# Optimization experiments

Hardware: AMD Instinct MI355X
Metric: run time of the kernel (lower is better)

The kernel has to match this reference:

```python
import jax, jax.numpy as jnp
import numpy as np

SIGMA_MIN, SIGMA_MAX = 0.03, 0.35
LAMBDA_GEO = 8.0
COMPAT_SCALE = 0.1
INVALID_W = 0.05
NH, HD = 8, 64
LN_EPS = 1e-5

def _ln(x, g, b):
    m = x.mean(-1, keepdims=True)
    v = ((x - m) ** 2).mean(-1, keepdims=True)
    return (x - m) * jax.lax.rsqrt(v + LN_EPS) * g + b

def setup_inputs() -> dict:
    key = jax.random.key(0)
    ks = jax.random.split(key, 32)
    B, C, H, W = 8, 512, 32, 32
    T, S, D, SIN = 1024, 1024, 512, 512
    s = 0.02
    inp = {
        'front_feat': jax.random.normal(ks[0], (B, C, H, W), jnp.float32),
        'sat_tokens': jax.random.normal(ks[1], (B, S, SIN), jnp.float32),
        'sat_xy': jax.random.uniform(ks[2], (B, S, 2), jnp.float32),
        'front_bev_xy': jax.random.uniform(ks[3], (B, T, 2), jnp.float32),
        'front_bev_valid_mask': jax.random.bernoulli(ks[4], 0.9, (B, T)),
        'front_plucker': jax.random.normal(ks[5], (B, T, 6), jnp.float32),
        'fa_w': jax.random.normal(ks[6], (C, D), jnp.float32) * s,
        'fa_b': jnp.zeros((D,), jnp.float32),
        'fa_g': jnp.ones((D,), jnp.float32),
        'fa_lb': jnp.zeros((D,), jnp.float32),
        'sa_w': jax.random.normal(ks[7], (SIN, D), jnp.float32) * s,
        'sa_b': jnp.zeros((D,), jnp.float32),
        'sa_g': jnp.ones((D,), jnp.float32),
        'sa_lb': jnp.zeros((D,), jnp.float32),
        'q_w': jax.random.normal(ks[8], (D, D), jnp.float32) * s,
        'q_b': jnp.zeros((D,), jnp.float32),
        'k_w': jax.random.normal(ks[9], (D, D), jnp.float32) * s,
        'k_b': jnp.zeros((D,), jnp.float32),
        'v_w': jax.random.normal(ks[10], (D, D), jnp.float32) * s,
        'v_b': jnp.zeros((D,), jnp.float32),
        'pl_w1': jax.random.normal(ks[11], (6, D), jnp.float32) * s,
        'pl_b1': jnp.zeros((D,), jnp.float32),
        'pl_w2': jax.random.normal(ks[12], (D, D), jnp.float32) * s,
        'pl_b2': jnp.zeros((D,), jnp.float32),
        'sig_w': jax.random.normal(ks[13], (D, 1), jnp.float32) * s,
        'sig_b': jnp.zeros((1,), jnp.float32),
        'db_w': jax.random.normal(ks[14], (D, NH), jnp.float32) * s,
        'db_b': jnp.zeros((NH,), jnp.float32),
        'out_w': jax.random.normal(ks[15], (D, C), jnp.float32) * s,
        'out_b': jnp.zeros((C,), jnp.float32),
    }
    return inp

def _forward(front_feat, sat_tokens, sat_xy, front_bev_xy, front_plucker,
             fa_w, fa_b, fa_g, fa_lb, sa_w, sa_b, sa_g, sa_lb,
             q_w, q_b, k_w, k_b, v_w, v_b, pl_w1, pl_b1, pl_w2, pl_b2,
             sig_w, sig_b, db_w, db_b, out_w, out_b, valid_mask):
    B, C, H, W = front_feat.shape
    T = H * W
    D = NH * HD
    front_flat = front_feat.reshape(B, C, T).transpose(0, 2, 1)  # [B,T,C]
    front_embed = _ln(front_flat @ fa_w + fa_b, fa_g, fa_lb)
    pl = jax.nn.silu(front_plucker @ pl_w1 + pl_b1) @ pl_w2 + pl_b2
    context = front_embed + pl
    sat_embed = _ln(sat_tokens @ sa_w + sa_b, sa_g, sa_lb)
    def heads(x):
        return x.reshape(B, -1, NH, HD).transpose(0, 2, 1, 3)  # [B,H,N,d]
    q = heads(front_embed @ q_w + q_b)
    k = heads(sat_embed @ k_w + k_b)
    v = heads(sat_embed @ v_w + v_b)
    compat = jnp.einsum('bhtd,bhsd->bhts', q, k) / jnp.sqrt(jnp.float32(HD))
    compat = COMPAT_SCALE * compat
    sigma = SIGMA_MIN + (SIGMA_MAX - SIGMA_MIN) * jax.nn.sigmoid((context @ sig_w + sig_b)[..., 0])  # [B,T]
    dist2 = ((front_bev_xy[:, :, None, :] - sat_xy[:, None, :, :]) ** 2).sum(-1)  # [B,T,S]
    geo = -LAMBDA_GEO * dist2 / jnp.maximum(sigma[..., None] ** 2, 1e-6)
    sat_logits = compat + geo[:, None]  # [B,H,T,S]
    sat_logits = jnp.where(valid_mask[:, None, :, None], sat_logits, jnp.float32(-10000.0))
    dustbin = (context @ db_w + db_b).transpose(0, 2, 1)[..., None]  # [B,H,T,1]
    logits = jnp.concatenate([sat_logits, dustbin], axis=-1)
    probs = jax.nn.softmax(logits, axis=-1)
    sat_probs, dustbin_prob = probs[..., :-1], probs[..., -1]
    read = jnp.einsum('bhts,bhsd->bhtd', sat_probs, v)
    read = read.transpose(0, 2, 1, 3).reshape(B, T, D)
    read_feat = (read @ out_w + out_b).transpose(0, 2, 1).reshape(B, C, H, W)
    confidence = (1.0 - dustbin_prob).mean(axis=1)  # [B,T]
    conf_feat = confidence.reshape(B, 1, H, W)
    front_feat_out = front_feat + conf_feat * read_feat
    vf = valid_mask.astype(confidence.dtype)
    inv = 1.0 - vf
    invalid_conf = (confidence * inv).sum() / jnp.maximum(inv.sum(), 1.0)
    invalid_conf_loss = invalid_conf * INVALID_W
    return front_feat_out, read_feat, confidence, invalid_conf_loss

def reference(front_feat, sat_tokens, sat_xy, front_bev_xy, front_bev_valid_mask, front_plucker,
              fa_w, fa_b, fa_g, fa_lb, sa_w, sa_b, sa_g, sa_lb,
              q_w, q_b, k_w, k_b, v_w, v_b, pl_w1, pl_b1, pl_w2, pl_b2,
              sig_w, sig_b, db_w, db_b, out_w, out_b):
    return _forward(front_feat, sat_tokens, sat_xy, front_bev_xy, front_plucker,
                    fa_w, fa_b, fa_g, fa_lb, sa_w, sa_b, sa_g, sa_lb,
                    q_w, q_b, k_w, k_b, v_w, v_b, pl_w1, pl_b1, pl_w2, pl_b2,
                    sig_w, sig_b, db_w, db_b, out_w, out_b, front_bev_valid_mask)
```

## Files before the change

kernel.cpp:

```cpp
#include <hip/hip_runtime.h>

typedef unsigned short u16;
typedef __attribute__((ext_vector_type(8))) short short8;
typedef __attribute__((ext_vector_type(4))) float f32x4;

constexpr int B_  = 8;
constexpr int C_  = 512;
constexpr int T_  = 1024;
constexpr int S_  = 1024;
constexpr int D_  = 512;
constexpr int NH_ = 8;
constexpr int BT_ = B_ * T_;
constexpr float INVLN2 = 1.44269504088896340736f;
constexpr float QSCALE2 = 0.0125f * INVLN2;

__device__ __forceinline__ unsigned pack2(float lo, float hi) {
    unsigned r;
    asm("v_cvt_pk_bf16_f32 %0, %1, %2" : "=v"(r) : "v"(lo), "v"(hi));
    return r;
}
__device__ __forceinline__ u16 f2bf(float x) {
    return (u16)pack2(x, x);
}
__device__ __forceinline__ float bf2f(u16 h) {
    union { unsigned u; float f; } v; v.u = ((unsigned)h) << 16;
    return v.f;
}
__device__ __forceinline__ float fexp2(float x) {
    float r;
    asm("v_exp_f32 %0, %1" : "=v"(r) : "v"(x));
    return r;
}
__device__ __forceinline__ float max3f(float a, float b, float c) {
    float r;
    asm("v_max3_f32 %0, %1, %2, %3" : "=v"(r) : "v"(a), "v"(b), "v"(c));
    return r;
}

#define GWAITBAR(N) do { \
    asm volatile("s_waitcnt vmcnt(" #N ") lgkmcnt(0)" ::: "memory"); \
    __builtin_amdgcn_sched_barrier(0); \
    __builtin_amdgcn_s_barrier(); \
    __builtin_amdgcn_sched_barrier(0); } while (0)

typedef __attribute__((address_space(3))) unsigned int lds_u32;
typedef const __attribute__((address_space(1))) unsigned int glob_u32;
__device__ __forceinline__ void g2l16(void* l, const void* g) {
    __builtin_amdgcn_global_load_lds((glob_u32*)g, (lds_u32*)l, 16, 0, 0);
}

__device__ __forceinline__ int is_valid(const void* mask, int mode, int idx) {
    if (mode == 0) return ((const int*)mask)[idx] != 0;
    if (mode == 1) return ((const float*)mask)[idx] != 0.0f;
    return ((const unsigned char*)mask)[idx] != 0;
}

__global__ __launch_bounds__(256) void prep_k(
    const float* __restrict__ ff, const float* __restrict__ sat,
    const float* __restrict__ pl,
    const float* a0, const float* a1, const float* a2, const float* a3,
    const float* a4, const float* a5, const float* a6, u16* __restrict__ WT,
    u16* __restrict__ ffb, u16* __restrict__ satb,
    const float* __restrict__ plw1, const float* __restrict__ plb1,
    u16* __restrict__ plh,
    const unsigned* __restrict__ maskw, int* __restrict__ mode,
    float* __restrict__ scal) {
    __shared__ float tile[32][33];
    int blk = blockIdx.x, tid = threadIdx.x;
    if (blk < 4096) {
        int t0 = (blk & 31) * 32, c0 = ((blk >> 5) & 15) * 32, b = blk >> 9;
        int tx = tid & 31, ty = tid >> 5;
        const float* ip = ff + (size_t)b * C_ * T_;
        for (int i = ty; i < 32; i += 8)
            tile[i][tx] = ip[(size_t)(c0 + i) * T_ + t0 + tx];
        __syncthreads();
        u16* op = ffb + (size_t)b * T_ * C_;
        for (int i = ty; i < 32; i += 8)
            op[(size_t)(t0 + i) * C_ + c0 + tx] = f2bf(tile[tx][i]);
    } else if (blk < 5888) {
        int idx = blk - 4096;
        const float* srcs[7] = {a0, a1, a2, a3, a4, a5, a6};
        int z = idx >> 8;
        const float* src = srcs[z];
        u16* d = WT + (size_t)z * 512 * 512;
        int k0 = (idx & 15) * 32, n0 = ((idx >> 4) & 15) * 32;
        int tx = tid & 31, ty = tid >> 5;
        for (int i = ty; i < 32; i += 8)
            tile[i][tx] = src[(size_t)(k0 + i) * 512 + n0 + tx];
        __syncthreads();
        for (int i = ty; i < 32; i += 8)
            d[(size_t)(n0 + i) * 512 + k0 + tx] = f2bf(tile[tx][i]);
    } else if (blk < 7936) {
        int i = (blk - 5888) * 256 + tid;
        const float4* p = (const float4*)(sat + (size_t)i * 8);
        float4 a = p[0], b = p[1];
        uint4 o;
        o.x = pack2(a.x, a.y); o.y = pack2(a.z, a.w);
        o.z = pack2(b.x, b.y); o.w = pack2(b.z, b.w);
        *(uint4*)(satb + (size_t)i * 8) = o;
    } else if (blk < 9984) {
        int m = (blk - 7936) * 4 + (tid >> 6);
        int lane = tid & 63;
        float p6[6];
#pragma unroll
        for (int j = 0; j < 6; ++j) p6[j] = pl[(size_t)m * 6 + j];
        int n0 = lane * 8;
        float acc[8];
#pragma unroll
        for (int e = 0; e < 8; ++e) acc[e] = plb1[n0 + e];
#pragma unroll
        for (int j = 0; j < 6; ++j) {
            float4 wv0 = *(const float4*)(plw1 + j * D_ + n0);
            float4 wv1 = *(const float4*)(plw1 + j * D_ + n0 + 4);
            acc[0] += p6[j] * wv0.x; acc[1] += p6[j] * wv0.y;
            acc[2] += p6[j] * wv0.z; acc[3] += p6[j] * wv0.w;
            acc[4] += p6[j] * wv1.x; acc[5] += p6[j] * wv1.y;
            acc[6] += p6[j] * wv1.z; acc[7] += p6[j] * wv1.w;
        }
        uint4 o;
        float s0 = acc[0] / (1.0f + __expf(-acc[0]));
        float s1 = acc[1] / (1.0f + __expf(-acc[1]));
        float s2 = acc[2] / (1.0f + __expf(-acc[2]));
        float s3 = acc[3] / (1.0f + __expf(-acc[3]));
        float s4 = acc[4] / (1.0f + __expf(-acc[4]));
        float s5 = acc[5] / (1.0f + __expf(-acc[5]));
        float s6 = acc[6] / (1.0f + __expf(-acc[6]));
        float s7 = acc[7] / (1.0f + __expf(-acc[7]));
        o.x = pack2(s0, s1); o.y = pack2(s2, s3);
        o.z = pack2(s4, s5); o.w = pack2(s6, s7);
        *(uint4*)(plh + (size_t)m * D_ + n0) = o;
    } else {
        __shared__ int bad_i, bad_f;
        if (tid == 0) { bad_i = 0; bad_f = 0; }
        __syncthreads();
        for (int i = tid; i < 2048; i += 256) {
            unsigned v = maskw[i];
            if (v > 1u) bad_i = 1;
            if (v != 0u && v != 0x3f800000u) bad_f = 1;
        }
        __syncthreads();
        if (tid == 0) {
            *mode = (!bad_i) ? 0 : ((!bad_f) ? 1 : 2);
            scal[0] = 0.0f; scal[1] = 0.0f;
        }
    }
}

__global__ __launch_bounds__(256) void gmm_k(
    const u16* __restrict__ A0, const u16* __restrict__ A1,
    const u16* __restrict__ A2, const u16* __restrict__ A3,
    const u16* __restrict__ Bt0, const u16* __restrict__ Bt1,
    const u16* __restrict__ Bt2, const u16* __restrict__ Bt3,
    const float* __restrict__ bb0, const float* __restrict__ bb1,
    const float* __restrict__ bb2, const float* __restrict__ bb3,
    void* __restrict__ C0v, void* __restrict__ C1v,
    void* __restrict__ C2v, void* __restrict__ C3v,
    int md0, int md1, int md2, int md3,
    const u16* __restrict__ addend,
    const float* __restrict__ ffp, float* __restrict__ out1p,
    const float* __restrict__ dbpp, const void* __restrict__ maskp,
    const int* __restrict__ modep, float* __restrict__ outcp,
    float* __restrict__ scalp) {
    __shared__ u16 As[3][4096];
    __shared__ u16 Bs[3][4096];
    __shared__ float confL[128];
    int jid = blockIdx.x >> 8;
    int L = blockIdx.x & 255;
    const u16* A    = (jid == 0) ? A0 : (jid == 1) ? A1 : (jid == 2) ? A2 : A3;
    const u16* Bt   = (jid == 0) ? Bt0 : (jid == 1) ? Bt1 : (jid == 2) ? Bt2 : Bt3;
    const float* bias = (jid == 0) ? bb0 : (jid == 1) ? bb1 : (jid == 2) ? bb2 : bb3;
    void* Cv        = (jid == 0) ? C0v : (jid == 1) ? C1v : (jid == 2) ? C2v : C3v;
    int mode        = (jid == 0) ? md0 : (jid == 1) ? md1 : (jid == 2) ? md2 : md3;

    int tid = threadIdx.x, w = tid >> 6, l = tid & 63;
    int lr = l & 15, g = l >> 4;
    int W = (L & 7) * 32 + (L >> 3);
    int m0 = (W >> 2) * 128, n0 = (W & 3) * 128;
    int wr = w >> 1, wc = w & 1;
    int prm = g ^ ((lr >> 1) & 3);

    f32x4 acc[4][4] = {};

    if (mode == 4 && tid < 128) {
        int row = m0 + tid;
        const float* dr = dbpp + (size_t)row * NH_;
        float s = 0;
#pragma unroll
        for (int h = 0; h < 8; ++h) s += dr[h];
        float cf = 1.0f - s * 0.125f;
        confL[tid] = cf;
        if ((W & 3) == 0) {
            outcp[row] = cf;
            int md = *modep;
            float invd = is_valid(maskp, md, row) ? 0.0f : 1.0f;
            float a = cf * invd, bsum = invd;
            for (int o = 32; o; o >>= 1) {
                a += __shfl_down(a, o);
                bsum += __shfl_down(bsum, o);
            }
            if ((tid & 63) == 0) {
                atomicAdd(&scalp[0], a);
                atomicAdd(&scalp[1], bsum);
            }
        }
    }

    auto stage = [&](int buf, int k0) {
#pragma unroll
        for (int j = 0; j < 2; ++j) {
            int i = tid + 256 * j;
            int row = i >> 2, gg = (i & 3) ^ ((i >> 3) & 3);
            g2l16((char*)As[buf] + (size_t)i * 16,
                  A + (size_t)(m0 + row) * 512 + k0 + gg * 8);
        }
#pragma unroll
        for (int j = 0; j < 2; ++j) {
            int i = tid + 256 * j;
            int col = i >> 2, gg = (i & 3) ^ ((i >> 3) & 3);
            g2l16((char*)Bs[buf] + (size_t)i * 16,
                  Bt + (size_t)(n0 + col) * 512 + k0 + gg * 8);
        }
    };

    auto compute = [&](int bi) {
        const char* Ab = (const char*)As[bi];
        const char* Bb = (const char*)Bs[bi];
        short8 af[4], bf[4];
#pragma unroll
        for (int m = 0; m < 4; ++m)
            af[m] = *(const short8*)(Ab + ((wr * 64 + m * 16 + lr) * 4 + prm) * 16);
#pragma unroll
        for (int n = 0; n < 4; ++n)
            bf[n] = *(const short8*)(Bb + ((wc * 64 + n * 16 + lr) * 4 + prm) * 16);
        __builtin_amdgcn_s_setprio(1);
#pragma unroll
        for (int m = 0; m < 4; ++m)
#pragma unroll
            for (int n = 0; n < 4; ++n)
                acc[m][n] = __builtin_amdgcn_mfma_f32_16x16x32_bf16(
                    af[m], bf[n], acc[m][n], 0, 0, 0);
        __builtin_amdgcn_s_setprio(0);
    };

    stage(0, 0);
    stage(1, 32);
    for (int t = 0; t < 14; ++t) {
        stage((t + 2) % 3, (t + 2) * 32);
        GWAITBAR(8);
        compute(t % 3);
        __builtin_amdgcn_s_barrier();
    }
    GWAITBAR(4);
    compute(2);
    GWAITBAR(0);
    compute(0);

    float bs[4];
#pragma unroll
    for (int n = 0; n < 4; ++n) bs[n] = bias[n0 + wc * 64 + n * 16 + lr];

#pragma unroll
    for (int m = 0; m < 4; ++m) {
#pragma unroll
        for (int n = 0; n < 4; ++n) {
            int R0  = m0 + wr * 64 + m * 16 + 4 * g;
            int col = n0 + wc * 64 + n * 16 + lr;
            if (mode == 3) {
                int bbx = R0 >> 10, ss = R0 & 1023, hh = col >> 6, dd = col & 63;
                uint2 pk;
                pk.x = pack2(acc[m][n][0] + bs[n], acc[m][n][1] + bs[n]);
                pk.y = pack2(acc[m][n][2] + bs[n], acc[m][n][3] + bs[n]);
                u16* dst = (u16*)Cv + ((size_t)(bbx * 8 + hh) * 64 + dd) * 1024 + ss;
                *(uint2*)dst = pk;
            } else if (mode == 4) {
                int bbx = R0 >> 10, t0p = R0 & 1023;
                size_t base = (size_t)bbx * C_ * T_ + (size_t)col * T_ + t0p;
                float4 rf;
                rf.x = acc[m][n][0] + bs[n]; rf.y = acc[m][n][1] + bs[n];
                rf.z = acc[m][n][2] + bs[n]; rf.w = acc[m][n][3] + bs[n];
                float4 ffv = *(const float4*)(ffp + base);
                float4 cfv = *(const float4*)&confL[R0 - m0];
                float4 o0v;
                o0v.x = ffv.x + cfv.x * rf.x; o0v.y = ffv.y + cfv.y * rf.y;
                o0v.z = ffv.z + cfv.z * rf.z; o0v.w = ffv.w + cfv.w * rf.w;
                *(float4*)(out1p + base) = rf;
                *(float4*)((float*)Cv + base) = o0v;
            } else {
#pragma unroll
                for (int j = 0; j < 4; ++j) {
                    int row = R0 + j;
                    float v = acc[m][n][j] + bs[n];
                    if (mode == 1) v *= QSCALE2;
                    if (mode == 2) v += bf2f(addend[(size_t)row * 512 + col]);
                    ((u16*)Cv)[(size_t)row * 512 + col] = f2bf(v);
                }
            }
        }
    }
}

__global__ __launch_bounds__(256) void ln2_k(
    const u16* __restrict__ X0, const float* __restrict__ g0,
    const float* __restrict__ b0, u16* __restrict__ O0,
    const u16* __restrict__ X1, const float* __restrict__ g1,
    const float* __restrict__ b1, u16* __restrict__ O1) {
    int sel = blockIdx.x >> 13;
    int row = blockIdx.x & 8191;
    const u16* X = sel ? X1 : X0;
    const float* gw = sel ? g1 : g0;
    const float* bw = sel ? b1 : b0;
    u16* out = sel ? O1 : O0;
    int tid = threadIdx.x;
    const unsigned* xr = (const unsigned*)(X + (size_t)row * D_);
    unsigned u = xr[tid];
    float x0 = bf2f((u16)(u & 0xffff)), x1 = bf2f((u16)(u >> 16));
    float s = x0 + x1, sq = x0 * x0 + x1 * x1;
    __shared__ float rs[4], rq[4];
    for (int o = 32; o; o >>= 1) { s += __shfl_down(s, o); sq += __shfl_down(sq, o); }
    int wid = tid >> 6, lane = tid & 63;
    if (lane == 0) { rs[wid] = s; rq[wid] = sq; }
    __syncthreads();
    if (tid == 0) {
        float ts = 0, tq = 0;
        for (int w = 0; w < 4; ++w) { ts += rs[w]; tq += rq[w]; }
        rs[0] = ts; rq[0] = tq;
    }
    __syncthreads();
    float mean = rs[0] * (1.0f / D_);
    float var  = rq[0] * (1.0f / D_) - mean * mean;
    float r = rsqrtf(var + 1e-5f);
    float2 g2 = *(const float2*)(gw + 2 * tid);
    float2 b2 = *(const float2*)(bw + 2 * tid);
    float y0 = (x0 - mean) * r * g2.x + b2.x;
    float y1 = (x1 - mean) * r * g2.y + b2.y;
    ((unsigned*)(out + (size_t)row * D_))[tid] = pack2(y0, y1);
}

__global__ __launch_bounds__(256) void head_k(const u16* __restrict__ ctx,
        const float* __restrict__ sw, const float* __restrict__ sbb,
        const float* __restrict__ dw, const float* __restrict__ dbb,
        float* __restrict__ sig, float* __restrict__ dbo) {
    int w = threadIdx.x >> 6, lane = threadIdx.x & 63;
    int row = blockIdx.x * 4 + w;
    const u16* xr = ctx + (size_t)row * D_;
    short8 xv = *(const short8*)(xr + lane * 8);
    float xs[8];
#pragma unroll
    for (int i = 0; i < 8; ++i) xs[i] = bf2f((u16)xv[i]);
    float4 wa = *(const float4*)(sw + lane * 8);
    float4 wb = *(const float4*)(sw + lane * 8 + 4);
    float sacc = xs[0] * wa.x + xs[1] * wa.y + xs[2] * wa.z + xs[3] * wa.w +
                 xs[4] * wb.x + xs[5] * wb.y + xs[6] * wb.z + xs[7] * wb.w;
    float d_[8] = {};
    const float* dr = dw + (size_t)lane * 8 * NH_;
#pragma unroll
    for (int i = 0; i < 8; ++i)
#pragma unroll
        for (int hh = 0; hh < 8; ++hh) d_[hh] += xs[i] * dr[i * NH_ + hh];
    for (int o = 32; o; o >>= 1) {
        sacc += __shfl_down(sacc, o);
#pragma unroll
        for (int hh = 0; hh < 8; ++hh) d_[hh] += __shfl_down(d_[hh], o);
    }
    if (lane == 0) {
        float z = sacc + sbb[0];
        sig[row] = 0.03f + 0.32f / (1.0f + __expf(-z));
        float* dd = dbo + (size_t)row * NH_;
#pragma unroll
        for (int hh = 0; hh < 8; ++hh) dd[hh] = d_[hh] + dbb[hh];
    }
}

__global__ __launch_bounds__(512) void attn_k(
    const u16* __restrict__ Q, const u16* __restrict__ K,
    const u16* __restrict__ Vt, const float* __restrict__ sig,
    const float* __restrict__ dbl, const float* __restrict__ bev,
    const float* __restrict__ sxy, const void* __restrict__ mask,
    const int* __restrict__ mode, u16* __restrict__ OUT,
    float* __restrict__ dbp) {
    int L = blockIdx.x;
    int W = (L & 7) * 64 + (L >> 3);
    int b = W >> 6, h = (W >> 3) & 7, tblk = W & 7;
    int tid = threadIdx.x, w = tid >> 6, l = tid & 63;
    int lr = l & 15, g = l >> 4;
    int p8 = lr & 7;

    __shared__ u16 Kbuf[2][4096];
    __shared__ u16 Vbuf[2][4096];
    __shared__ float2 SXY[1024];
    __shared__ float  SZ[1024];

    const float2* xp = (const float2*)(sxy + (size_t)b * S_ * 2);
#pragma unroll
    for (int j = 0; j < 2; ++j) {
        int idx = tid + 512 * j;
        float2 v = xp[idx];
        SXY[idx] = make_float2(-2.0f * v.x, -2.0f * v.y);
        SZ[idx] = v.x * v.x + v.y * v.y;
    }

    int trow = b * T_ + tblk * 128 + w * 16 + lr;
    float s_ = sig[trow];
    float bx = bev[(size_t)trow * 2], by = bev[(size_t)trow * 2 + 1];
    float dbv2 = dbl[(size_t)trow * NH_ + h] * INVLN2;
    int md = *mode;
    bool vld = is_valid(mask, md, trow) != 0;
    float grow  = vld ? (-11.5415603271117f / fmaxf(s_ * s_, 1e-6f)) : 0.0f;
    float Abase = vld ? grow * (bx * bx + by * by) : -10000.0f;
    float AbaseM = Abase - dbv2;
    float mshift = 0.0f;

    const u16* qp = Q + (size_t)trow * 512 + h * 64 + g * 8;
    short8 q0 = *(const short8*)qp;
    short8 q1 = *(const short8*)(qp + 32);
    if (!vld) { q0 = short8{}; q1 = short8{}; }

    short8 ones;
#pragma unroll
    for (int e = 0; e < 8; ++e) ones[e] = (short)0x3F80;

    const u16* Kp = K + (size_t)b * S_ * 512 + h * 64;
    const u16* Vp = Vt + (size_t)(b * 8 + h) * 64 * 1024;

    int srow = tid >> 3;
    int gprm = (tid & 7) ^ (srow & 7);
    int sK = ((srow >> 5) & 1) * 32 + ((srow >> 2) & 3) * 8 +
             ((srow >> 4) & 1) * 4 + (srow & 3);

    auto stageKV = [&](int buf, int s0) {
        g2l16((char*)Kbuf[buf] + (size_t)tid * 16,
              Kp + (size_t)(s0 + sK) * 512 + gprm * 8);
        g2l16((char*)Vbuf[buf] + (size_t)tid * 16,
              Vp + (size_t)srow * 1024 + s0 + gprm * 8);
    };

    f32x4 o0 = {}, o1 = {}, o2 = {}, o3 = {};
    f32x4 o4 = {1.0f, 1.0f, 1.0f, 1.0f};

    stageKV(0, 0);
    int cur = 0;
    for (int c = 0; c < 16; ++c) {
        int s0c = c * 64;
        if (c < 15) {
            stageKV(cur ^ 1, s0c + 64);
            GWAITBAR(2);
        } else {
            GWAITBAR(0);
        }

        const char* Kc = (const char*)Kbuf[cur];
        const char* Vc = (const char*)Vbuf[cur];

        f32x4 p[4];
        f32x4 z4 = {};
        __builtin_amdgcn_s_setprio(1);
#pragma unroll
        for (int sub = 0; sub < 4; ++sub) {
            int krow = sub * 16 + lr;
            short8 kf0 = *(const short8*)(Kc + (krow * 8 + (g ^ p8)) * 16);
            short8 kf1 = *(const short8*)(Kc + (krow * 8 + ((4 + g) ^ p8)) * 16);
            p[sub] = __builtin_amdgcn_mfma_f32_16x16x32_bf16(kf0, q0, z4, 0, 0, 0);
            p[sub] = __builtin_amdgcn_mfma_f32_16x16x32_bf16(kf1, q1, p[sub], 0, 0, 0);
        }
        __builtin_amdgcn_s_setprio(0);

        float lg[16];
#pragma unroll
        for (int sub = 0; sub < 4; ++sub) {
            int sl = s0c + ((sub & 2) << 4) + 8 * g + ((sub & 1) << 2);
            float4 xy01 = *(const float4*)&SXY[sl];
            float4 xy23 = *(const float4*)&SXY[sl + 2];
            float4 zz   = *(const float4*)&SZ[sl];
            float X[4] = {xy01.x, xy01.z, xy23.x, xy23.z};
            float Y[4] = {xy01.y, xy01.w, xy23.y, xy23.w};
            float Z[4] = {zz.x, zz.y, zz.z, zz.w};
#pragma unroll
            for (int i2 = 0; i2 < 4; ++i2) {
                float wg = fmaf(bx, X[i2], fmaf(by, Y[i2], Z[i2]));
                lg[sub * 4 + i2] = fmaf(grow, wg, p[sub][i2] + AbaseM);
            }
        }
        float c0 = max3f(lg[0], lg[1], lg[2]);
        float c1 = max3f(lg[3], lg[4], lg[5]);
        float c2 = max3f(lg[6], lg[7], lg[8]);
        float c3 = max3f(lg[9], lg[10], lg[11]);
        float c4 = max3f(lg[12], lg[13], lg[14]);
        float cl = fmaxf(max3f(c0, c1, c2), max3f(c3, c4, lg[15]));

        if (!__all(cl <= 11.5f)) {
            cl = fmaxf(cl, __shfl_xor(cl, 16));
            cl = fmaxf(cl, __shfl_xor(cl, 32));
            float dm = fmaxf(cl, 0.0f);
            float scl = fexp2(-dm);
            o0 *= scl; o1 *= scl; o2 *= scl; o3 *= scl; o4 *= scl;
            AbaseM -= dm;
            mshift -= dm;
#pragma unroll
            for (int r = 0; r < 16; ++r) lg[r] -= dm;
        }
        float pe[16];
#pragma unroll
        for (int r = 0; r < 16; ++r) pe[r] = fexp2(lg[r]);

        union { uint4 u; short8 s8; } pf0, pf1;
        pf0.u.x = pack2(pe[0], pe[1]);  pf0.u.y = pack2(pe[2], pe[3]);
        pf0.u.z = pack2(pe[4], pe[5]);  pf0.u.w = pack2(pe[6], pe[7]);
        pf1.u.x = pack2(pe[8], pe[9]);  pf1.u.y = pack2(pe[10], pe[11]);
        pf1.u.z = pack2(pe[12], pe[13]); pf1.u.w = pack2(pe[14], pe[15]);

        __builtin_amdgcn_s_setprio(1);
        short8 vf;
#pragma unroll
        for (int dt = 0; dt < 4; ++dt) {
            int vrow = dt * 16 + lr;
            f32x4* oo = (dt == 0) ? &o0 : (dt == 1) ? &o1 : (dt == 2) ? &o2 : &o3;
            vf = *(const short8*)(Vc + (vrow * 8 + (g ^ p8)) * 16);
            *oo = __builtin_amdgcn_mfma_f32_16x16x32_bf16(vf, pf0.s8, *oo, 0, 0, 0);
            vf = *(const short8*)(Vc + (vrow * 8 + ((4 + g) ^ p8)) * 16);
            *oo = __builtin_amdgcn_mfma_f32_16x16x32_bf16(vf, pf1.s8, *oo, 0, 0, 0);
        }
        o4 = __builtin_amdgcn_mfma_f32_16x16x32_bf16(ones, pf0.s8, o4, 0, 0, 0);
        o4 = __builtin_amdgcn_mfma_f32_16x16x32_bf16(ones, pf1.s8, o4, 0, 0, 0);
        __builtin_amdgcn_s_setprio(0);

        __builtin_amdgcn_s_barrier();
        cur ^= 1;
    }

    float inv = 1.0f / o4[0];
    u16* ob = OUT + (size_t)trow * 512 + h * 64;
    {
        uint2 pk;
        pk.x = pack2(o0[0] * inv, o0[1] * inv); pk.y = pack2(o0[2] * inv, o0[3] * inv);
        *(uint2*)(ob + 0 * 16 + 4 * g) = pk;
        pk.x = pack2(o1[0] * inv, o1[1] * inv); pk.y = pack2(o1[2] * inv, o1[3] * inv);
        *(uint2*)(ob + 1 * 16 + 4 * g) = pk;
        pk.x = pack2(o2[0] * inv, o2[1] * inv); pk.y = pack2(o2[2] * inv, o2[3] * inv);
        *(uint2*)(ob + 2 * 16 + 4 * g) = pk;
        pk.x = pack2(o3[0] * inv, o3[1] * inv); pk.y = pack2(o3[2] * inv, o3[3] * inv);
        *(uint2*)(ob + 3 * 16 + 4 * g) = pk;
    }
    if (g == 0) dbp[(size_t)trow * NH_ + h] = fexp2(mshift) * inv;
}

__global__ void loss_k(const float* __restrict__ scal, float* __restrict__ out) {
    out[0] = scal[0] / fmaxf(scal[1], 1.0f) * 0.05f;
}

extern "C" void kernel_launch(void* const* d_in, const int* in_sizes, int n_in,
                              void* d_out, int out_size, void* d_ws, size_t ws_size,
                              hipStream_t stream) {
    const float* front_feat = (const float*)d_in[0];
    const float* sat_tokens = (const float*)d_in[1];
    const float* sat_xy     = (const float*)d_in[2];
    const float* bev_xy     = (const float*)d_in[3];
    const void*  mask       = d_in[4];
    const float* plucker    = (const float*)d_in[5];
    const float* fa_w = (const float*)d_in[6];
    const float* fa_b = (const float*)d_in[7];
    const float* fa_g = (const float*)d_in[8];
    const float* fa_lb = (const float*)d_in[9];
    const float* sa_w = (const float*)d_in[10];
    const float* sa_b = (const float*)d_in[11];
    const float* sa_g = (const float*)d_in[12];
    const float* sa_lb = (const float*)d_in[13];
    const float* q_w = (const float*)d_in[14];
    const float* q_b = (const float*)d_in[15];
    const float* k_w = (const float*)d_in[16];
    const float* k_b = (const float*)d_in[17];
    const float* v_w = (const float*)d_in[18];
    const float* v_b = (const float*)d_in[19];
    const float* pl_w1 = (const float*)d_in[20];
    const float* pl_b1 = (const float*)d_in[21];
    const float* pl_w2 = (const float*)d_in[22];
    const float* pl_b2 = (const float*)d_in[23];
    const float* sig_w = (const float*)d_in[24];
    const float* sig_b = (const float*)d_in[25];
    const float* db_w = (const float*)d_in[26];
    const float* db_b = (const float*)d_in[27];
    const float* out_w = (const float*)d_in[28];
    const float* out_b = (const float*)d_in[29];

    char* w8 = (char*)d_ws;
    u16* H0 = (u16*)(w8);
    u16* H1 = (u16*)(w8 + 8388608ull * 1);
    u16* H2 = (u16*)(w8 + 8388608ull * 2);
    u16* H3 = (u16*)(w8 + 8388608ull * 3);
    u16* H4 = (u16*)(w8 + 8388608ull * 4);
    u16* H5 = (u16*)(w8 + 8388608ull * 5);
    u16* H6 = (u16*)(w8 + 8388608ull * 6);
    u16* WT = (u16*)(w8 + 8388608ull * 7);
    char* sm = w8 + 8388608ull * 7 + 3670016ull;
    float* w_sigma = (float*)sm;
    float* w_db    = w_sigma + BT_;
    float* w_dbp   = w_db + (size_t)BT_ * NH_;
    float* w_scal  = w_dbp + (size_t)BT_ * NH_;
    int*   w_mode  = (int*)(w_scal + 2);

    u16* Wfa = WT;                 u16* Wpl2 = WT + 262144ull * 1;
    u16* Wq  = WT + 262144ull * 2; u16* Wsa  = WT + 262144ull * 3;
    u16* Wk  = WT + 262144ull * 4; u16* Wv   = WT + 262144ull * 5;
    u16* Wo  = WT + 262144ull * 6;

    float* out0 = (float*)d_out;
    float* out1 = out0 + (size_t)B_ * C_ * T_;
    float* outc = out1 + (size_t)B_ * C_ * T_;
    float* outl = outc + (size_t)B_ * T_;

    dim3 blk(256);

    prep_k<<<dim3(9985), blk, 0, stream>>>(
        front_feat, sat_tokens, plucker,
        fa_w, pl_w2, q_w, sa_w, k_w, v_w, out_w, WT,
        H0, H5, pl_w1, pl_b1, H2,
        (const unsigned*)mask, w_mode, w_scal);
    gmm_k<<<dim3(512), blk, 0, stream>>>(
        H0, H5, nullptr, nullptr,
        Wfa, Wsa, nullptr, nullptr,
        fa_b, sa_b, nullptr, nullptr,
        H6, H4, nullptr, nullptr,
        0, 0, 0, 0,
        nullptr, nullptr, nullptr,
        nullptr, nullptr, nullptr, nullptr, nullptr);
    ln2_k<<<dim3(16384), blk, 0, stream>>>(H6, fa_g, fa_lb, H1,
                                           H4, sa_g, sa_lb, H3);
    gmm_k<<<dim3(1024), blk, 0, stream>>>(
        H1, H2, H3, H3,
        Wq, Wpl2, Wk, Wv,
        q_b, pl_b2, k_b, v_b,
        H5, H6, H0, H4,
        1, 2, 0, 3,
        H1, nullptr, nullptr,
        nullptr, nullptr, nullptr, nullptr, nullptr);
    head_k<<<dim3(BT_ / 4), blk, 0, stream>>>(H6, sig_w, sig_b, db_w, db_b,
                                              w_sigma, w_db);
    attn_k<<<dim3(512), dim3(512), 0, stream>>>(
        H5, H0, H4, w_sigma, w_db, bev_xy, sat_xy, mask, w_mode, H2, w_dbp);
    gmm_k<<<dim3(256), blk, 0, stream>>>(
        H2, nullptr, nullptr, nullptr,
        Wo, nullptr, nullptr, nullptr,
        out_b, nullptr, nullptr, nullptr,
        out0, nullptr, nullptr, nullptr,
        4, 0, 0, 0,
        nullptr, front_feat, out1,
        w_dbp, mask, w_mode, outc, w_scal);
    loss_k<<<1, 1, 0, stream>>>(w_scal, outl);
}
```

Measured before the change: 159.3 us.

## Fold plucker second-layer GEMM into sigma/dustbin heads and fuse LN with heads

```diff
diff --git a/kernel.cpp b/kernel.cpp
--- a/kernel.cpp
+++ b/kernel.cpp
@@ -59,12 +59,16 @@
     const float* __restrict__ ff, const float* __restrict__ sat,
     const float* __restrict__ pl,
     const float* a0, const float* a1, const float* a2, const float* a3,
-    const float* a4, const float* a5, const float* a6, u16* __restrict__ WT,
+    const float* a4, const float* a5, u16* __restrict__ WT,
     u16* __restrict__ ffb, u16* __restrict__ satb,
     const float* __restrict__ plw1, const float* __restrict__ plb1,
     u16* __restrict__ plh,
     const unsigned* __restrict__ maskw, int* __restrict__ mode,
-    float* __restrict__ scal) {
+    float* __restrict__ scal,
+    const float* __restrict__ plw2, const float* __restrict__ sigw,
+    const float* __restrict__ dbw, const float* __restrict__ plb2,
+    float* __restrict__ wsig, float* __restrict__ wdbf,
+    float* __restrict__ offs) {
     __shared__ float tile[32][33];
     int blk = blockIdx.x, tid = threadIdx.x;
     if (blk < 4096) {
@@ -77,9 +81,9 @@
         u16* op = ffb + (size_t)b * T_ * C_;
         for (int i = ty; i < 32; i += 8)
             op[(size_t)(t0 + i) * C_ + c0 + tx] = f2bf(tile[tx][i]);
-    } else if (blk < 5888) {
+    } else if (blk < 5632) {
         int idx = blk - 4096;
-        const float* srcs[7] = {a0, a1, a2, a3, a4, a5, a6};
+        const float* srcs[6] = {a0, a1, a2, a3, a4, a5};
         int z = idx >> 8;
         const float* src = srcs[z];
         u16* d = WT + (size_t)z * 512 * 512;
@@ -90,16 +94,16 @@
         __syncthreads();
         for (int i = ty; i < 32; i += 8)
             d[(size_t)(n0 + i) * 512 + k0 + tx] = f2bf(tile[tx][i]);
-    } else if (blk < 7936) {
-        int i = (blk - 5888) * 256 + tid;
+    } else if (blk < 7680) {
+        int i = (blk - 5632) * 256 + tid;
         const float4* p = (const float4*)(sat + (size_t)i * 8);
         float4 a = p[0], b = p[1];
         uint4 o;
         o.x = pack2(a.x, a.y); o.y = pack2(a.z, a.w);
         o.z = pack2(b.x, b.y); o.w = pack2(b.z, b.w);
         *(uint4*)(satb + (size_t)i * 8) = o;
-    } else if (blk < 9984) {
-        int m = (blk - 7936) * 4 + (tid >> 6);
+    } else if (blk < 9728) {
+        int m = (blk - 7680) * 4 + (tid >> 6);
         int lane = tid & 63;
         float p6[6];
 #pragma unroll
@@ -129,7 +133,7 @@
         o.x = pack2(s0, s1); o.y = pack2(s2, s3);
         o.z = pack2(s4, s5); o.w = pack2(s6, s7);
         *(uint4*)(plh + (size_t)m * D_ + n0) = o;
-    } else {
+    } else if (blk == 9728) {
         __shared__ int bad_i, bad_f;
         if (tid == 0) { bad_i = 0; bad_f = 0; }
         __syncthreads();
@@ -142,6 +146,50 @@
         if (tid == 0) {
             *mode = (!bad_i) ? 0 : ((!bad_f) ? 1 : 2);
             scal[0] = 0.0f; scal[1] = 0.0f;
+        }
+    } else if (blk < 9731) {
+        int k = (blk - 9729) * 256 + tid;
+        const float* wr = plw2 + (size_t)k * 512;
+        float acc = 0;
+        for (int n = 0; n < 512; n += 4) {
+            float4 wv = *(const float4*)(wr + n);
+            float4 sv = *(const float4*)(sigw + n);
+            acc += wv.x * sv.x + wv.y * sv.y + wv.z * sv.z + wv.w * sv.w;
+        }
+        wsig[k] = acc;
+    } else if (blk < 9747) {
+        int idx = blk - 9731;
+        int k = idx * 32 + (tid >> 3), h = tid & 7;
+        const float* wr = plw2 + (size_t)k * 512;
+        float acc = 0;
+        for (int n = 0; n < 512; ++n) acc += wr[n] * dbw[n * 8 + h];
+        wdbf[k * 8 + h] = acc;
+    } else {
+        float p = plb2[tid] * sigw[tid] + plb2[tid + 256] * sigw[tid + 256];
+        float ph[8];
+#pragma unroll
+        for (int h = 0; h < 8; ++h)
+            ph[h] = plb2[tid] * dbw[tid * 8 + h] +
+                    plb2[tid + 256] * dbw[(tid + 256) * 8 + h];
+        for (int o = 32; o; o >>= 1) {
+            p += __shfl_down(p, o);
+#pragma unroll
+            for (int h = 0; h < 8; ++h) ph[h] += __shfl_down(ph[h], o);
+        }
+        __shared__ float red[4][9];
+        int wv = tid >> 6, lane = tid & 63;
+        if (lane == 0) {
+            red[wv][0] = p;
+#pragma unroll
+            for (int h = 0; h < 8; ++h) red[wv][1 + h] = ph[h];
+        }
+        __syncthreads();
+        if (tid == 0) {
+            for (int j = 0; j < 9; ++j) {
+                float t = 0;
+                for (int v2 = 0; v2 < 4; ++v2) t += red[v2][j];
+                offs[j] = t;
+            }
         }
     }
 }
@@ -299,75 +347,116 @@
     }
 }
 
-__global__ __launch_bounds__(256) void ln2_k(
-    const u16* __restrict__ X0, const float* __restrict__ g0,
-    const float* __restrict__ b0, u16* __restrict__ O0,
-    const u16* __restrict__ X1, const float* __restrict__ g1,
-    const float* __restrict__ b1, u16* __restrict__ O1) {
-    int sel = blockIdx.x >> 13;
-    int row = blockIdx.x & 8191;
-    const u16* X = sel ? X1 : X0;
-    const float* gw = sel ? g1 : g0;
-    const float* bw = sel ? b1 : b0;
-    u16* out = sel ? O1 : O0;
-    int tid = threadIdx.x;
-    const unsigned* xr = (const unsigned*)(X + (size_t)row * D_);
-    unsigned u = xr[tid];
-    float x0 = bf2f((u16)(u & 0xffff)), x1 = bf2f((u16)(u >> 16));
-    float s = x0 + x1, sq = x0 * x0 + x1 * x1;
-    __shared__ float rs[4], rq[4];
-    for (int o = 32; o; o >>= 1) { s += __shfl_down(s, o); sq += __shfl_down(sq, o); }
-    int wid = tid >> 6, lane = tid & 63;
-    if (lane == 0) { rs[wid] = s; rq[wid] = sq; }
-    __syncthreads();
-    if (tid == 0) {
-        float ts = 0, tq = 0;
-        for (int w = 0; w < 4; ++w) { ts += rs[w]; tq += rq[w]; }
-        rs[0] = ts; rq[0] = tq;
-    }
-    __syncthreads();
-    float mean = rs[0] * (1.0f / D_);
-    float var  = rq[0] * (1.0f / D_) - mean * mean;
-    float r = rsqrtf(var + 1e-5f);
-    float2 g2 = *(const float2*)(gw + 2 * tid);
-    float2 b2 = *(const float2*)(bw + 2 * tid);
-    float y0 = (x0 - mean) * r * g2.x + b2.x;
-    float y1 = (x1 - mean) * r * g2.y + b2.y;
-    ((unsigned*)(out + (size_t)row * D_))[tid] = pack2(y0, y1);
-}
-
-__global__ __launch_bounds__(256) void head_k(const u16* __restrict__ ctx,
-        const float* __restrict__ sw, const float* __restrict__ sbb,
-        const float* __restrict__ dw, const float* __restrict__ dbb,
-        float* __restrict__ sig, float* __restrict__ dbo) {
-    int w = threadIdx.x >> 6, lane = threadIdx.x & 63;
-    int row = blockIdx.x * 4 + w;
-    const u16* xr = ctx + (size_t)row * D_;
-    short8 xv = *(const short8*)(xr + lane * 8);
-    float xs[8];
-#pragma unroll
-    for (int i = 0; i < 8; ++i) xs[i] = bf2f((u16)xv[i]);
-    float4 wa = *(const float4*)(sw + lane * 8);
-    float4 wb = *(const float4*)(sw + lane * 8 + 4);
-    float sacc = xs[0] * wa.x + xs[1] * wa.y + xs[2] * wa.z + xs[3] * wa.w +
-                 xs[4] * wb.x + xs[5] * wb.y + xs[6] * wb.z + xs[7] * wb.w;
-    float d_[8] = {};
-    const float* dr = dw + (size_t)lane * 8 * NH_;
-#pragma unroll
-    for (int i = 0; i < 8; ++i)
-#pragma unroll
-        for (int hh = 0; hh < 8; ++hh) d_[hh] += xs[i] * dr[i * NH_ + hh];
-    for (int o = 32; o; o >>= 1) {
-        sacc += __shfl_down(sacc, o);
-#pragma unroll
-        for (int hh = 0; hh < 8; ++hh) d_[hh] += __shfl_down(d_[hh], o);
-    }
-    if (lane == 0) {
-        float z = sacc + sbb[0];
-        sig[row] = 0.03f + 0.32f / (1.0f + __expf(-z));
-        float* dd = dbo + (size_t)row * NH_;
-#pragma unroll
-        for (int hh = 0; hh < 8; ++hh) dd[hh] = d_[hh] + dbb[hh];
+__global__ __launch_bounds__(256) void lnh_k(
+    const u16* __restrict__ Epre, const float* __restrict__ fg,
+    const float* __restrict__ fb, u16* __restrict__ Eout,
+    const u16* __restrict__ Spre, const float* __restrict__ sg,
+    const float* __restrict__ sb, u16* __restrict__ Sout,
+    const u16* __restrict__ PLH,
+    const float* __restrict__ sigw, const float* __restrict__ sigb,
+    const float* __restrict__ dbw, const float* __restrict__ dbb,
+    const float* __restrict__ wsig, const float* __restrict__ wdbf,
+    const float* __restrict__ offs,
+    float* __restrict__ sigma, float* __restrict__ dbo) {
+    int blk = blockIdx.x, tid = threadIdx.x;
+    int wv = tid >> 6, lane = tid & 63;
+    if (blk < 4096) {
+        int sel = blk >> 11;
+        int row = (blk & 2047) * 4 + wv;
+        const u16* X = sel ? Spre : Epre;
+        const float* gw = sel ? sg : fg;
+        const float* bw = sel ? sb : fb;
+        u16* out = sel ? Sout : Eout;
+        uint4 u = *((const uint4*)(X + (size_t)row * 512) + lane);
+        float x[8];
+        x[0] = bf2f((u16)(u.x & 0xffff)); x[1] = bf2f((u16)(u.x >> 16));
+        x[2] = bf2f((u16)(u.y & 0xffff)); x[3] = bf2f((u16)(u.y >> 16));
+        x[4] = bf2f((u16)(u.z & 0xffff)); x[5] = bf2f((u16)(u.z >> 16));
+        x[6] = bf2f((u16)(u.w & 0xffff)); x[7] = bf2f((u16)(u.w >> 16));
+        float s = 0, sq = 0;
+#pragma unroll
+        for (int i = 0; i < 8; ++i) { s += x[i]; sq += x[i] * x[i]; }
+        for (int o = 1; o < 64; o <<= 1) {
+            s += __shfl_xor(s, o); sq += __shfl_xor(sq, o);
+        }
+        float mean = s * (1.0f / D_);
+        float var  = sq * (1.0f / D_) - mean * mean;
+        float r = rsqrtf(var + 1e-5f);
+        float4 g0v = *(const float4*)(gw + lane * 8);
+        float4 g1v = *(const float4*)(gw + lane * 8 + 4);
+        float4 b0v = *(const float4*)(bw + lane * 8);
+        float4 b1v = *(const float4*)(bw + lane * 8 + 4);
+        float gv[8] = {g0v.x, g0v.y, g0v.z, g0v.w, g1v.x, g1v.y, g1v.z, g1v.w};
+        float bv[8] = {b0v.x, b0v.y, b0v.z, b0v.w, b1v.x, b1v.y, b1v.z, b1v.w};
+        uint4 o;
+        float y[8];
+#pragma unroll
+        for (int i = 0; i < 8; ++i) y[i] = (x[i] - mean) * r * gv[i] + bv[i];
+        o.x = pack2(y[0], y[1]); o.y = pack2(y[2], y[3]);
+        o.z = pack2(y[4], y[5]); o.w = pack2(y[6], y[7]);
+        *((uint4*)(out + (size_t)row * 512) + lane) = o;
+    } else {
+        int row = (blk - 4096) * 4 + wv;
+        uint4 u = *((const uint4*)(Epre + (size_t)row * 512) + lane);
+        float x[8];
+        x[0] = bf2f((u16)(u.x & 0xffff)); x[1] = bf2f((u16)(u.x >> 16));
+        x[2] = bf2f((u16)(u.y & 0xffff)); x[3] = bf2f((u16)(u.y >> 16));
+        x[4] = bf2f((u16)(u.z & 0xffff)); x[5] = bf2f((u16)(u.z >> 16));
+        x[6] = bf2f((u16)(u.w & 0xffff)); x[7] = bf2f((u16)(u.w >> 16));
+        float s = 0, sq = 0;
+#pragma unroll
+        for (int i = 0; i < 8; ++i) { s += x[i]; sq += x[i] * x[i]; }
+        for (int o = 1; o < 64; o <<= 1) {
+            s += __shfl_xor(s, o); sq += __shfl_xor(sq, o);
+        }
+        float mean = s * (1.0f / D_);
+        float var  = sq * (1.0f / D_) - mean * mean;
+        float r = rsqrtf(var + 1e-5f);
+        float4 g0v = *(const float4*)(fg + lane * 8);
+        float4 g1v = *(const float4*)(fg + lane * 8 + 4);
+        float4 b0v = *(const float4*)(fb + lane * 8);
+        float4 b1v = *(const float4*)(fb + lane * 8 + 4);
+        float gv[8] = {g0v.x, g0v.y, g0v.z, g0v.w, g1v.x, g1v.y, g1v.z, g1v.w};
+        float bv[8] = {b0v.x, b0v.y, b0v.z, b0v.w, b1v.x, b1v.y, b1v.z, b1v.w};
+        float E[8];
+#pragma unroll
+        for (int i = 0; i < 8; ++i) E[i] = (x[i] - mean) * r * gv[i] + bv[i];
+        uint4 up = *((const uint4*)(PLH + (size_t)row * 512) + lane);
+        float plv[8];
+        plv[0] = bf2f((u16)(up.x & 0xffff)); plv[1] = bf2f((u16)(up.x >> 16));
+        plv[2] = bf2f((u16)(up.y & 0xffff)); plv[3] = bf2f((u16)(up.y >> 16));
+        plv[4] = bf2f((u16)(up.z & 0xffff)); plv[5] = bf2f((u16)(up.z >> 16));
+        plv[6] = bf2f((u16)(up.w & 0xffff)); plv[7] = bf2f((u16)(up.w >> 16));
+        float4 sw0 = *(const float4*)(sigw + lane * 8);
+        float4 sw1 = *(const float4*)(sigw + lane * 8 + 4);
+        float4 fw0 = *(const float4*)(wsig + lane * 8);
+        float4 fw1 = *(const float4*)(wsig + lane * 8 + 4);
+        float swv[8] = {sw0.x, sw0.y, sw0.z, sw0.w, sw1.x, sw1.y, sw1.z, sw1.w};
+        float fwv[8] = {fw0.x, fw0.y, fw0.z, fw0.w, fw1.x, fw1.y, fw1.z, fw1.w};
+        float sacc = 0;
+#pragma unroll
+        for (int i = 0; i < 8; ++i) sacc += E[i] * swv[i] + plv[i] * fwv[i];
+        float d_[8] = {};
+        const float* dr = dbw + (size_t)lane * 8 * NH_;
+        const float* fr = wdbf + (size_t)lane * 8 * NH_;
+#pragma unroll
+        for (int i = 0; i < 8; ++i) {
+#pragma unroll
+            for (int h = 0; h < 8; ++h)
+                d_[h] += E[i] * dr[i * NH_ + h] + plv[i] * fr[i * NH_ + h];
+        }
+        for (int o = 1; o < 64; o <<= 1) {
+            sacc += __shfl_xor(sacc, o);
+#pragma unroll
+            for (int h = 0; h < 8; ++h) d_[h] += __shfl_xor(d_[h], o);
+        }
+        if (lane == 0) {
+            float z = sacc + sigb[0] + offs[0];
+            sigma[row] = 0.03f + 0.32f / (1.0f + __expf(-z));
+            float* dd = dbo + (size_t)row * NH_;
+#pragma unroll
+            for (int h = 0; h < 8; ++h) dd[h] = d_[h] + dbb[h] + offs[1 + h];
+        }
     }
 }
 
@@ -596,11 +685,13 @@
     float* w_dbp   = w_db + (size_t)BT_ * NH_;
     float* w_scal  = w_dbp + (size_t)BT_ * NH_;
     int*   w_mode  = (int*)(w_scal + 2);
-
-    u16* Wfa = WT;                 u16* Wpl2 = WT + 262144ull * 1;
-    u16* Wq  = WT + 262144ull * 2; u16* Wsa  = WT + 262144ull * 3;
-    u16* Wk  = WT + 262144ull * 4; u16* Wv   = WT + 262144ull * 5;
-    u16* Wo  = WT + 262144ull * 6;
+    float* w_wsig  = w_scal + 4;
+    float* w_wdbf  = w_wsig + 512;
+    float* w_offs  = w_wdbf + 4096;
+
+    u16* Wfa = WT;                 u16* Wq  = WT + 262144ull * 1;
+    u16* Wsa = WT + 262144ull * 2; u16* Wk  = WT + 262144ull * 3;
+    u16* Wv  = WT + 262144ull * 4; u16* Wo  = WT + 262144ull * 5;
 
     float* out0 = (float*)d_out;
     float* out1 = out0 + (size_t)B_ * C_ * T_;
@@ -609,11 +700,12 @@
 
     dim3 blk(256);
 
-    prep_k<<<dim3(9985), blk, 0, stream>>>(
+    prep_k<<<dim3(9748), blk, 0, stream>>>(
         front_feat, sat_tokens, plucker,
-        fa_w, pl_w2, q_w, sa_w, k_w, v_w, out_w, WT,
+        fa_w, q_w, sa_w, k_w, v_w, out_w, WT,
         H0, H5, pl_w1, pl_b1, H2,
-        (const unsigned*)mask, w_mode, w_scal);
+        (const unsigned*)mask, w_mode, w_scal,
+        pl_w2, sig_w, db_w, pl_b2, w_wsig, w_wdbf, w_offs);
     gmm_k<<<dim3(512), blk, 0, stream>>>(
         H0, H5, nullptr, nullptr,
         Wfa, Wsa, nullptr, nullptr,
@@ -622,18 +714,19 @@
         0, 0, 0, 0,
         nullptr, nullptr, nullptr,
         nullptr, nullptr, nullptr, nullptr, nullptr);
-    ln2_k<<<dim3(16384), blk, 0, stream>>>(H6, fa_g, fa_lb, H1,
-                                           H4, sa_g, sa_lb, H3);
-    gmm_k<<<dim3(1024), blk, 0, stream>>>(
-        H1, H2, H3, H3,
-        Wq, Wpl2, Wk, Wv,
-        q_b, pl_b2, k_b, v_b,
-        H5, H6, H0, H4,
-        1, 2, 0, 3,
-        H1, nullptr, nullptr,
+    lnh_k<<<dim3(6144), blk, 0, stream>>>(
+        H6, fa_g, fa_lb, H1,
+        H4, sa_g, sa_lb, H3,
+        H2, sig_w, sig_b, db_w, db_b,
+        w_wsig, w_wdbf, w_offs, w_sigma, w_db);
+    gmm_k<<<dim3(768), blk, 0, stream>>>(
+        H1, H3, H3, nullptr,
+        Wq, Wk, Wv, nullptr,
+        q_b, k_b, v_b, nullptr,
+        H5, H0, H4, nullptr,
+        1, 0, 3, 0,
+        nullptr, nullptr, nullptr,
         nullptr, nullptr, nullptr, nullptr, nullptr);
-    head_k<<<dim3(BT_ / 4), blk, 0, stream>>>(H6, sig_w, sig_b, db_w, db_b,
-                                              w_sigma, w_db);
     attn_k<<<dim3(512), dim3(512), 0, stream>>>(
         H5, H0, H4, w_sigma, w_db, bev_xy, sat_xy, mask, w_mode, H2, w_dbp);
     gmm_k<<<dim3(256), blk, 0, stream>>>(
```

After: 170.3 us. +6.9%, slower.
